# Optimization experiments

Hardware: AMD Instinct MI355X
Metric: run time of the kernel (lower is better)

The kernel has to match this reference:

```python
import jax, jax.numpy as jnp
import numpy as np

D_K = 64

def setup_inputs() -> dict:
    key = jax.random.key(0)
    kq, kk, kv = jax.random.split(key, 3)
    B, Lq, Lk, d = 32, 2048, 2048, D_K
    return {
        "query": jax.random.normal(kq, (B, Lq, d), dtype=jnp.float32),
        "key": jax.random.normal(kk, (B, Lk, d), dtype=jnp.float32),
        "value": jax.random.normal(kv, (B, Lk, d), dtype=jnp.float32),
    }

def reference(query, key, value):
    d_k = query.shape[-1]
    scale = 1.0 / jnp.sqrt(jnp.asarray(d_k, query.dtype))
    scores = jnp.einsum('nqd,nkd->nqk', query, key) * scale  # (B, Lq, Lk)
    attn = jax.nn.softmax(scores, axis=-1)  # masked=None -> plain softmax; dropout p=0.0 is identity
    return jnp.einsum('nqk,nkd->nqd', attn, value)  # (B, Lq, d_v)
```

## Files before the change

### kernel.cpp

```cpp
#include <hip/hip_runtime.h>


#define NB   32
#define LSEQ 2048
#define DH   64
#define BM   64
#define BN   64
#define NIT  (LSEQ / BN)

typedef __attribute__((ext_vector_type(8)))  __bf16 bf16x8;
typedef __attribute__((ext_vector_type(16))) float  f32x16;
typedef __attribute__((ext_vector_type(2)))  unsigned uint2v;

union BF8 { bf16x8 v; unsigned short u[8]; unsigned u32[4]; uint4 q; };

__device__ __forceinline__ unsigned short f2bf(float f) {
    unsigned int u = __builtin_bit_cast(unsigned int, f);
    u += 0x7fffu + ((u >> 16) & 1u);
    return (unsigned short)(u >> 16);
}

__device__ __forceinline__ unsigned pack_bf2(float a, float b) {
    unsigned ua = __builtin_bit_cast(unsigned, a) + 0x8000u;
    unsigned ub = __builtin_bit_cast(unsigned, b) + 0x8000u;
    return __builtin_amdgcn_perm(ub, ua, 0x07060302u);
}

__device__ __forceinline__ float fast_exp2(float x) {
#if __has_builtin(__builtin_amdgcn_exp2f)
    return __builtin_amdgcn_exp2f(x);
#else
    return exp2f(x);
#endif
}

__device__ __forceinline__ void load_lds16(const void* g, void* l) {
    __builtin_amdgcn_global_load_lds(
        (const __attribute__((address_space(1))) void*)g,
        (__attribute__((address_space(3))) void*)l, 16, 0, 0);
}

#define KBLK ((NB * LSEQ * 8) / 256)
__global__ __launch_bounds__(256)
void prep(const float* __restrict__ Kg, const float* __restrict__ Vg,
          unsigned short* __restrict__ Kb, unsigned short* __restrict__ Vt) {
    __shared__ __align__(16) unsigned T2[64 * 36];
    const int tid = threadIdx.x;
    if (blockIdx.x < KBLK) {
        const int CH  = blockIdx.x * 256 + tid;
        const int b   = CH >> 14;
        const int rem = CH & 16383;
        const int n   = rem >> 3;
        const int cc  = rem & 7;
        const int c   = cc ^ (n & 7);
        const float* src = Kg + (((size_t)b * LSEQ + n) * DH + c * 8);
        float4 f0 = ((const float4*)src)[0];
        float4 f1 = ((const float4*)src)[1];
        BF8 t;
        t.u[0]=f2bf(f0.x); t.u[1]=f2bf(f0.y); t.u[2]=f2bf(f0.z); t.u[3]=f2bf(f0.w);
        t.u[4]=f2bf(f1.x); t.u[5]=f2bf(f1.y); t.u[6]=f2bf(f1.z); t.u[7]=f2bf(f1.w);
        *(bf16x8*)&Kb[(size_t)CH * 8] = t.v;
    } else {
        const int bx = blockIdx.x - KBLK;
        const int b  = bx >> 5;
        const int nt = bx & 31;
        const int n  = (tid >> 3) * 2;
        const int dc = (tid & 7) * 8;
        const float* s0 = Vg + (((size_t)b * LSEQ + nt * 64 + n) * DH + dc);
        float4 a0 = ((const float4*)s0)[0];
        float4 a1 = ((const float4*)s0)[1];
        const float* s1 = s0 + DH;
        float4 b0 = ((const float4*)s1)[0];
        float4 b1 = ((const float4*)s1)[1];
        float va[8] = {a0.x,a0.y,a0.z,a0.w, a1.x,a1.y,a1.z,a1.w};
        float vb[8] = {b0.x,b0.y,b0.z,b0.w, b1.x,b1.y,b1.z,b1.w};
        const int n2 = n >> 1;
        #pragma unroll
        for (int j = 0; j < 8; ++j)
            T2[(dc + j) * 36 + n2] = (unsigned)f2bf(va[j]) | ((unsigned)f2bf(vb[j]) << 16);
        __syncthreads();
        #pragma unroll
        for (int i = 0; i < 2; ++i) {
            const int CH = i * 256 + tid;
            const int cc = CH >> 6;
            const int d  = CH & 63;
            uint4 o = *(const uint4*)&T2[d * 36 + cc * 4];
            *(uint4*)&Vt[((((size_t)(b * 32 + nt)) * 8 + cc) * 64 + d) * 8] = o;
        }
    }
}

__global__ __launch_bounds__(256, 4)
void attn_fwd(const unsigned short* __restrict__ Kb,
              const unsigned short* __restrict__ Vt,
              const float* __restrict__ Qg,
              float* __restrict__ Og) {
    __shared__ __align__(16) char smem[18944];
    unsigned short* Kl = (unsigned short*)smem;
    float* Mrg = (float*)smem;
    float* Lsh = (float*)(smem + 18432);

    const int tid  = threadIdx.x;
    const int wave = tid >> 6;
    const int lane = tid & 63;
    const int m32  = lane & 31;
    const int h    = lane >> 5;
    const int qh   = wave >> 1;
    const int kvh  = wave & 1;

    const int L  = blockIdx.y * 32 + blockIdx.x;
    const int Lp = (L & 7) * 128 + (L >> 3);
    const int b  = Lp >> 5;
    const int qt = Lp & 31;

    const float qscale = 0.18033688011112042f;
    const int qrow = qt * BM + qh * 32 + m32;
    bf16x8 qf[4];
    {
        const float* qp = Qg + ((size_t)(b * LSEQ + qrow)) * DH;
        #pragma unroll
        for (int kt = 0; kt < 4; ++kt) {
            const float* p4 = qp + kt * 16 + h * 8;
            float4 f0 = ((const float4*)p4)[0];
            float4 f1 = ((const float4*)p4)[1];
            BF8 t;
            t.u[0]=f2bf(f0.x*qscale); t.u[1]=f2bf(f0.y*qscale);
            t.u[2]=f2bf(f0.z*qscale); t.u[3]=f2bf(f0.w*qscale);
            t.u[4]=f2bf(f1.x*qscale); t.u[5]=f2bf(f1.y*qscale);
            t.u[6]=f2bf(f1.z*qscale); t.u[7]=f2bf(f1.w*qscale);
            qf[kt] = t.v;
        }
    }

    int kidx[4];
    #pragma unroll
    for (int kt = 0; kt < 4; ++kt) {
        const int n  = kvh * 32 + m32;
        const int cc = kt * 2 + h;
        kidx[kt] = (n * 8 + (cc ^ (n & 7))) * 8;
    }

    const char* vgb = (const char*)Vt + (size_t)b * (32 * 8 * 64 * 16);
    const int v00 = (((kvh * 4 + 0 + h) * 64) +  0 + m32) * 16;
    const int v01 = (((kvh * 4 + 2 + h) * 64) +  0 + m32) * 16;
    const int v10 = (((kvh * 4 + 0 + h) * 64) + 32 + m32) * 16;
    const int v11 = (((kvh * 4 + 2 + h) * 64) + 32 + m32) * 16;

    const char* kgb = (const char*)Kb + (size_t)b * (LSEQ * DH * 2);
    const int CH0 = wave * 128 + lane;
    const int CH1 = CH0 + 64;

    {
        char* kd = smem + wave * 2048;
        load_lds16(kgb + CH0 * 16, kd);
        load_lds16(kgb + CH1 * 16, kd + 1024);
    }

    f32x16 o0, o1;
    #pragma unroll
    for (int i = 0; i < 16; ++i) { o0[i] = 0.f; o1[i] = 0.f; }
    float l_run = 0.f;

    for (int nt = 0; nt < NIT; ++nt) {
        const int cur = nt & 1;
        __syncthreads();

        BF8 vf00, vf01, vf10, vf11;
        {
            const char* vp = vgb + nt * 8192;
            vf00.q = *(const uint4*)(vp + v00);
            vf01.q = *(const uint4*)(vp + v01);
            vf10.q = *(const uint4*)(vp + v10);
            vf11.q = *(const uint4*)(vp + v11);
        }

        if (nt + 1 < NIT) {
            char* kd = smem + (cur ^ 1) * 8192 + wave * 2048;
            load_lds16(kgb + (nt + 1) * 8192 + CH0 * 16, kd);
            load_lds16(kgb + (nt + 1) * 8192 + CH1 * 16, kd + 1024);
        }

        const unsigned short* kb = Kl + cur * 4096;
        f32x16 s;
        #pragma unroll
        for (int i = 0; i < 16; ++i) s[i] = 0.f;
        __builtin_amdgcn_s_setprio(1);
        #pragma unroll
        for (int kt = 0; kt < 4; ++kt) {
            bf16x8 kf = *(const bf16x8*)&kb[kidx[kt]];
            s = __builtin_amdgcn_mfma_f32_32x32x16_bf16(kf, qf[kt], s, 0, 0, 0);
        }
        __builtin_amdgcn_s_setprio(0);

        unsigned pk[8];
        #pragma unroll
        for (int g = 0; g < 4; ++g) {
            float e0 = fast_exp2(s[4*g]);
            float e1 = fast_exp2(s[4*g+1]);
            float e2 = fast_exp2(s[4*g+2]);
            float e3 = fast_exp2(s[4*g+3]);
            l_run += ((e0 + e1) + (e2 + e3));
            pk[2*g]   = pack_bf2(e0, e1);
            pk[2*g+1] = pack_bf2(e2, e3);
        }

        BF8 p0, p1;
#if __has_builtin(__builtin_amdgcn_permlane32_swap)
        {
            uint2v r;
            r = __builtin_amdgcn_permlane32_swap(pk[0], pk[2], false, false);
            p0.u32[0] = r[0]; p0.u32[2] = r[1];
            r = __builtin_amdgcn_permlane32_swap(pk[1], pk[3], false, false);
            p0.u32[1] = r[0]; p0.u32[3] = r[1];
            r = __builtin_amdgcn_permlane32_swap(pk[4], pk[6], false, false);
            p1.u32[0] = r[0]; p1.u32[2] = r[1];
            r = __builtin_amdgcn_permlane32_swap(pk[5], pk[7], false, false);
            p1.u32[1] = r[0]; p1.u32[3] = r[1];
        }
#else
        {
            const unsigned sA0 = h ? pk[0] : pk[2];
            const unsigned sA1 = h ? pk[1] : pk[3];
            const unsigned sB0 = h ? pk[4] : pk[6];
            const unsigned sB1 = h ? pk[5] : pk[7];
            const unsigned rA0 = __shfl_xor((int)sA0, 32, 64);
            const unsigned rA1 = __shfl_xor((int)sA1, 32, 64);
            const unsigned rB0 = __shfl_xor((int)sB0, 32, 64);
            const unsigned rB1 = __shfl_xor((int)sB1, 32, 64);
            p0.u32[0] = h ? rA0 : pk[0];  p0.u32[1] = h ? rA1 : pk[1];
            p0.u32[2] = h ? pk[2] : rA0;  p0.u32[3] = h ? pk[3] : rA1;
            p1.u32[0] = h ? rB0 : pk[4];  p1.u32[1] = h ? rB1 : pk[5];
            p1.u32[2] = h ? pk[6] : rB0;  p1.u32[3] = h ? pk[7] : rB1;
        }
#endif

        __builtin_amdgcn_s_setprio(1);
        o0 = __builtin_amdgcn_mfma_f32_32x32x16_bf16(vf00.v, p0.v, o0, 0, 0, 0);
        o0 = __builtin_amdgcn_mfma_f32_32x32x16_bf16(vf01.v, p1.v, o0, 0, 0, 0);
        o1 = __builtin_amdgcn_mfma_f32_32x32x16_bf16(vf10.v, p0.v, o1, 0, 0, 0);
        o1 = __builtin_amdgcn_mfma_f32_32x32x16_bf16(vf11.v, p1.v, o1, 0, 0, 0);
        __builtin_amdgcn_s_setprio(0);
    }

    const float l2 = l_run + __shfl_xor(l_run, 32, 64);
    __syncthreads();
    if (kvh) {
        float* mp = Mrg + ((size_t)qh * 64 + lane) * 36;
        #pragma unroll
        for (int g = 0; g < 4; ++g) {
            *(float4*)(mp + 4*g)      = (float4){o0[4*g], o0[4*g+1], o0[4*g+2], o0[4*g+3]};
            *(float4*)(mp + 16 + 4*g) = (float4){o1[4*g], o1[4*g+1], o1[4*g+2], o1[4*g+3]};
        }
        if (h == 0) Lsh[qh * 32 + m32] = l2;
    }
    __syncthreads();
    if (!kvh) {
        const float* mp = Mrg + ((size_t)qh * 64 + lane) * 36;
        #pragma unroll
        for (int g = 0; g < 4; ++g) {
            float4 a = *(const float4*)(mp + 4*g);
            float4 c = *(const float4*)(mp + 16 + 4*g);
            o0[4*g] += a.x; o0[4*g+1] += a.y; o0[4*g+2] += a.z; o0[4*g+3] += a.w;
            o1[4*g] += c.x; o1[4*g+1] += c.y; o1[4*g+2] += c.z; o1[4*g+3] += c.w;
        }
        const float inv = 1.0f / (l2 + Lsh[qh * 32 + m32]);
        float* op = Og + ((size_t)(b * LSEQ + qrow)) * DH;
        #pragma unroll
        for (int t = 0; t < 2; ++t)
            #pragma unroll
            for (int g = 0; g < 4; ++g) {
                float4 v;
                v.x = (t ? o1[4*g+0] : o0[4*g+0]) * inv;
                v.y = (t ? o1[4*g+1] : o0[4*g+1]) * inv;
                v.z = (t ? o1[4*g+2] : o0[4*g+2]) * inv;
                v.w = (t ? o1[4*g+3] : o0[4*g+3]) * inv;
                *(float4*)(op + t * 32 + g * 8 + h * 4) = v;
            }
    }
}

extern "C" void kernel_launch(void* const* d_in, const int* in_sizes, int n_in,
                              void* d_out, int out_size, void* d_ws, size_t ws_size,
                              hipStream_t stream) {
    const float* Q = (const float*)d_in[0];
    const float* K = (const float*)d_in[1];
    const float* V = (const float*)d_in[2];
    float* O = (float*)d_out;

    unsigned short* Kb = (unsigned short*)d_ws;
    unsigned short* Vt = (unsigned short*)d_ws + 4u * 1024u * 1024u;

    prep<<<dim3(KBLK + NB * (LSEQ / 64)), dim3(256), 0, stream>>>(K, V, Kb, Vt);
    attn_fwd<<<dim3(LSEQ / BM, NB), dim3(256), 0, stream>>>(Kb, Vt, Q, O);
}
```

Measured before the change: 137.2 us.

## Widen K prep to two chunks per thread, pad V transpose, use native bf16 pack

The K-conversion part of the prep kernel now has each thread handle two 8-element chunks, loading 64 contiguous bytes of a row and writing two swizzled bf16 vectors. This halves the number of K blocks and gives each thread wider loads. The V transpose buffer stride changes from 36 to 33 words to cut LDS bank conflicts, at the cost of unaligned scalar LDS reads. In the attention loop, the manual round-and-perm bf16 pack is replaced with compiler bf16 conversion, which may map to a native packed convert. The first MFMA now reads from a zero vector instead of zeroing the score accumulator each iteration, and the shuffle fallback for permlane32_swap is removed.

```diff
diff --git a/kernel.cpp b/kernel.cpp
--- a/kernel.cpp
+++ b/kernel.cpp
@@ -20,10 +20,10 @@
     return (unsigned short)(u >> 16);
 }
 
-__device__ __forceinline__ unsigned pack_bf2(float a, float b) {
-    unsigned ua = __builtin_bit_cast(unsigned, a) + 0x8000u;
-    unsigned ub = __builtin_bit_cast(unsigned, b) + 0x8000u;
-    return __builtin_amdgcn_perm(ub, ua, 0x07060302u);
+__device__ __forceinline__ unsigned cvt_pk_bf16(float a, float b) {
+    union { __bf16 h[2]; unsigned u; } t;
+    t.h[0] = (__bf16)a; t.h[1] = (__bf16)b;
+    return t.u;
 }
 
 __device__ __forceinline__ float fast_exp2(float x) {
@@ -40,28 +40,39 @@
         (__attribute__((address_space(3))) void*)l, 16, 0, 0);
 }
 
-#define KBLK ((NB * LSEQ * 8) / 256)
+#define KPB 1024
 __global__ __launch_bounds__(256)
 void prep(const float* __restrict__ Kg, const float* __restrict__ Vg,
           unsigned short* __restrict__ Kb, unsigned short* __restrict__ Vt) {
-    __shared__ __align__(16) unsigned T2[64 * 36];
+    __shared__ __align__(16) unsigned T2[64 * 33];
     const int tid = threadIdx.x;
-    if (blockIdx.x < KBLK) {
-        const int CH  = blockIdx.x * 256 + tid;
-        const int b   = CH >> 14;
-        const int rem = CH & 16383;
-        const int n   = rem >> 3;
-        const int cc  = rem & 7;
-        const int c   = cc ^ (n & 7);
-        const float* src = Kg + (((size_t)b * LSEQ + n) * DH + c * 8);
+    if (blockIdx.x < KPB) {
+        const int CP   = blockIdx.x * 256 + tid;
+        const int b    = CP >> 13;
+        const int rem  = CP & 8191;
+        const int n    = rem >> 2;
+        const int ccp  = rem & 3;
+        const int c0   = (ccp * 2) ^ (n & 7);
+        const int base = c0 & ~1;
+        const int sw   = c0 & 1;
+        const float* src = Kg + (((size_t)b * LSEQ + n) * DH + base * 8);
         float4 f0 = ((const float4*)src)[0];
         float4 f1 = ((const float4*)src)[1];
-        BF8 t;
-        t.u[0]=f2bf(f0.x); t.u[1]=f2bf(f0.y); t.u[2]=f2bf(f0.z); t.u[3]=f2bf(f0.w);
-        t.u[4]=f2bf(f1.x); t.u[5]=f2bf(f1.y); t.u[6]=f2bf(f1.z); t.u[7]=f2bf(f1.w);
-        *(bf16x8*)&Kb[(size_t)CH * 8] = t.v;
+        float4 f2 = ((const float4*)src)[2];
+        float4 f3 = ((const float4*)src)[3];
+        float c[16] = {f0.x,f0.y,f0.z,f0.w, f1.x,f1.y,f1.z,f1.w,
+                       f2.x,f2.y,f2.z,f2.w, f3.x,f3.y,f3.z,f3.w};
+        BF8 lo, hi;
+        #pragma unroll
+        for (int j = 0; j < 8; ++j) {
+            lo.u[j] = f2bf(c[sw * 8 + j]);
+            hi.u[j] = f2bf(c[(sw ^ 1) * 8 + j]);
+        }
+        unsigned short* dst = Kb + (((size_t)b * LSEQ + n) * 8 + ccp * 2) * 8;
+        *(bf16x8*)dst       = lo.v;
+        *(bf16x8*)(dst + 8) = hi.v;
     } else {
-        const int bx = blockIdx.x - KBLK;
+        const int bx = blockIdx.x - KPB;
         const int b  = bx >> 5;
         const int nt = bx & 31;
         const int n  = (tid >> 3) * 2;
@@ -77,14 +88,15 @@
         const int n2 = n >> 1;
         #pragma unroll
         for (int j = 0; j < 8; ++j)
-            T2[(dc + j) * 36 + n2] = (unsigned)f2bf(va[j]) | ((unsigned)f2bf(vb[j]) << 16);
+            T2[(dc + j) * 33 + n2] = (unsigned)f2bf(va[j]) | ((unsigned)f2bf(vb[j]) << 16);
         __syncthreads();
         #pragma unroll
         for (int i = 0; i < 2; ++i) {
             const int CH = i * 256 + tid;
             const int cc = CH >> 6;
             const int d  = CH & 63;
-            uint4 o = *(const uint4*)&T2[d * 36 + cc * 4];
+            const unsigned* tp = &T2[d * 33 + cc * 4];
+            uint4 o = { tp[0], tp[1], tp[2], tp[3] };
             *(uint4*)&Vt[((((size_t)(b * 32 + nt)) * 8 + cc) * 64 + d) * 8] = o;
         }
     }
@@ -156,9 +168,9 @@
         load_lds16(kgb + CH1 * 16, kd + 1024);
     }
 
-    f32x16 o0, o1;
+    f32x16 o0, o1, fz;
     #pragma unroll
-    for (int i = 0; i < 16; ++i) { o0[i] = 0.f; o1[i] = 0.f; }
+    for (int i = 0; i < 16; ++i) { o0[i] = 0.f; o1[i] = 0.f; fz[i] = 0.f; }
     float l_run = 0.f;
 
     for (int nt = 0; nt < NIT; ++nt) {
@@ -181,12 +193,11 @@
         }
 
         const unsigned short* kb = Kl + cur * 4096;
-        f32x16 s;
-        #pragma unroll
-        for (int i = 0; i < 16; ++i) s[i] = 0.f;
         __builtin_amdgcn_s_setprio(1);
-        #pragma unroll
-        for (int kt = 0; kt < 4; ++kt) {
+        bf16x8 kf0 = *(const bf16x8*)&kb[kidx[0]];
+        f32x16 s = __builtin_amdgcn_mfma_f32_32x32x16_bf16(kf0, qf[0], fz, 0, 0, 0);
+        #pragma unroll
+        for (int kt = 1; kt < 4; ++kt) {
             bf16x8 kf = *(const bf16x8*)&kb[kidx[kt]];
             s = __builtin_amdgcn_mfma_f32_32x32x16_bf16(kf, qf[kt], s, 0, 0, 0);
         }
@@ -200,12 +211,11 @@
             float e2 = fast_exp2(s[4*g+2]);
             float e3 = fast_exp2(s[4*g+3]);
             l_run += ((e0 + e1) + (e2 + e3));
-            pk[2*g]   = pack_bf2(e0, e1);
-            pk[2*g+1] = pack_bf2(e2, e3);
+            pk[2*g]   = cvt_pk_bf16(e0, e1);
+            pk[2*g+1] = cvt_pk_bf16(e2, e3);
         }
 
         BF8 p0, p1;
-#if __has_builtin(__builtin_amdgcn_permlane32_swap)
         {
             uint2v r;
             r = __builtin_amdgcn_permlane32_swap(pk[0], pk[2], false, false);
@@ -217,22 +227,6 @@
             r = __builtin_amdgcn_permlane32_swap(pk[5], pk[7], false, false);
             p1.u32[1] = r[0]; p1.u32[3] = r[1];
         }
-#else
-        {
-            const unsigned sA0 = h ? pk[0] : pk[2];
-            const unsigned sA1 = h ? pk[1] : pk[3];
-            const unsigned sB0 = h ? pk[4] : pk[6];
-            const unsigned sB1 = h ? pk[5] : pk[7];
-            const unsigned rA0 = __shfl_xor((int)sA0, 32, 64);
-            const unsigned rA1 = __shfl_xor((int)sA1, 32, 64);
-            const unsigned rB0 = __shfl_xor((int)sB0, 32, 64);
-            const unsigned rB1 = __shfl_xor((int)sB1, 32, 64);
-            p0.u32[0] = h ? rA0 : pk[0];  p0.u32[1] = h ? rA1 : pk[1];
-            p0.u32[2] = h ? pk[2] : rA0;  p0.u32[3] = h ? pk[3] : rA1;
-            p1.u32[0] = h ? rB0 : pk[4];  p1.u32[1] = h ? rB1 : pk[5];
-            p1.u32[2] = h ? pk[6] : rB0;  p1.u32[3] = h ? pk[7] : rB1;
-        }
-#endif
 
         __builtin_amdgcn_s_setprio(1);
         o0 = __builtin_amdgcn_mfma_f32_32x32x16_bf16(vf00.v, p0.v, o0, 0, 0, 0);
@@ -290,6 +284,6 @@
     unsigned short* Kb = (unsigned short*)d_ws;
     unsigned short* Vt = (unsigned short*)d_ws + 4u * 1024u * 1024u;
 
-    prep<<<dim3(KBLK + NB * (LSEQ / 64)), dim3(256), 0, stream>>>(K, V, Kb, Vt);
+    prep<<<dim3(KPB + NB * (LSEQ / 64)), dim3(256), 0, stream>>>(K, V, Kb, Vt);
     attn_fwd<<<dim3(LSEQ / BM, NB), dim3(256), 0, stream>>>(Kb, Vt, Q, O);
 }
```

Measured after the change: 138.3 us. No clear change (+0.8%).
